# Kernel tuning notes

Hardware: AMD Instinct MI355X
Metric: run time of the kernel (lower is better)

The kernel has to match this reference:

```python
import jax, jax.numpy as jnp
import numpy as np

B, IN_C, L, D, K, DEPTH, OUT = 16, 3, 2048, 256, 8, 4, 1
F = L // 2 + 1
EPS = 1e-5


def _hilbert_basis_rfft(grid_size, k):
    # Hilbert matrix Z[i,j] = 1/(i+j+1), symmetric PSD; take top-k eigvecs.
    i = np.arange(grid_size, dtype=np.float64)
    Z = 1.0 / (i[:, None] + i[None, :] + 1.0)
    w, V = np.linalg.eigh(Z)
    idx = np.argsort(w)[::-1][:k]
    Vt = V.T[idx]                                   # (k, L)
    Phi_f = np.fft.rfft(Vt, n=grid_size, axis=-1)   # (k, L//2+1) complex
    return Phi_f.astype(np.complex64)


def setup_inputs() -> dict:
    key = jax.random.key(0)
    ks = jax.random.split(key, 10)
    phi = _hilbert_basis_rfft(L, K)
    s = 0.05
    return {
        "x": jax.random.normal(ks[0], (B, IN_C, L), jnp.float32),
        "lift_w": jax.random.normal(ks[1], (D, IN_C + 1), jnp.float32) * s,
        "lift_b": jax.random.normal(ks[2], (D,), jnp.float32) * s,
        "theta": jax.random.normal(ks[3], (DEPTH, K, D, D), jnp.float32) * (1.0 / np.sqrt(D)),
        "ln_gamma": jnp.ones((DEPTH, D), jnp.float32),
        "ln_beta": jnp.zeros((DEPTH, D), jnp.float32),
        "glu_val_w": jax.random.normal(ks[4], (DEPTH, D, D), jnp.float32) * (1.0 / np.sqrt(D)),
        "glu_val_b": jax.random.normal(ks[5], (DEPTH, D), jnp.float32) * s,
        "glu_gate_w": jax.random.normal(ks[6], (DEPTH, D, D), jnp.float32) * (1.0 / np.sqrt(D)),
        "glu_gate_b": jax.random.normal(ks[7], (DEPTH, D), jnp.float32) * s,
        "head_w": jax.random.normal(ks[8], (OUT, D), jnp.float32) * (1.0 / np.sqrt(D)),
        "head_b": jax.random.normal(ks[9], (OUT,), jnp.float32) * s,
        "phi_real": jnp.asarray(phi.real, jnp.float32),
        "phi_imag": jnp.asarray(phi.imag, jnp.float32),
    }


def _layernorm_channels(h, gamma, beta):
    # h: (b, d, t); normalize over channel dim d (matches LayerNorm on transposed input)
    mu = jnp.mean(h, axis=1, keepdims=True)
    var = jnp.mean(jnp.square(h - mu), axis=1, keepdims=True)
    z = (h - mu) * jax.lax.rsqrt(var + EPS)
    return z * gamma[None, :, None] + beta[None, :, None]


def reference(x, lift_w, lift_b, theta, ln_gamma, ln_beta,
              glu_val_w, glu_val_b, glu_gate_w, glu_gate_b,
              head_w, head_b, phi_real, phi_imag):
    phi = phi_real + 1j * phi_imag                      # (K, F) complex
    phi_c = jnp.conj(phi)
    # add grid coordinate channel
    coords = jnp.linspace(0.0, 1.0, L, dtype=x.dtype)
    coords = jnp.broadcast_to(coords[None, None, :], (x.shape[0], 1, L))
    h = jnp.concatenate([x, coords], axis=1)            # (b, in+1, L)
    # pointwise lift (Conv1d kernel_size=1, norm=Identity)
    h = jnp.einsum("oi,bit->bot", lift_w, h) + lift_b[None, :, None]
    for i in range(DEPTH):
        z = _layernorm_channels(h, ln_gamma[i], ln_beta[i])
        Xf = jnp.fft.rfft(z, axis=-1)                   # (b, d, F) complex64
        # Exploit FFT linearity: S = sum_{l,d} Theta[l,h,d] * irfft(Xf[b,d] * conj(Phi[l]))
        #                          = irfft( sum_{l,d} Theta[l,h,d]*conj(Phi[l,f]) * Xf[b,d,f] )
        W = jnp.einsum("lhd,lf->hdf", theta[i].astype(Xf.dtype), phi_c)  # (h, d, F)
        Sf = jnp.einsum("bdf,hdf->bhf", Xf, W)          # (b, h, F)
        S = jnp.fft.irfft(Sf, n=L, axis=-1)             # (b, h, L)
        V = jnp.einsum("od,bdt->bot", glu_val_w[i], S) + glu_val_b[i][None, :, None]
        G = jax.nn.sigmoid(jnp.einsum("od,bdt->bot", glu_gate_w[i], S) + glu_gate_b[i][None, :, None])
        h = h + V * G                                   # residual + GLU
    y = jnp.einsum("od,bdt->bot", head_w, h) + head_b[None, :, None]
    return y
```

## Files before the change

kernel.cpp:

```cpp
#include <hip/hip_runtime.h>
#include <math.h>

#define NB 16
#define CIN 3
#define LL 2048
#define DD 256
#define KK 8
#define NDEPTH 4
#define FF 1025
#define FFP 1032
#define FFS 1032
#define LOGL 11

typedef _Float16 half8 __attribute__((ext_vector_type(8)));
typedef _Float16 half2v __attribute__((ext_vector_type(2)));
typedef float f32x4 __attribute__((ext_vector_type(4)));

union H8 { half8 h8; unsigned int u[4]; uint4 q; };
union H2 { _Float16 h[2]; unsigned int u; half2v v; };
union PK4 { float2 f2[4]; uint4 q[2]; };

#if defined(__has_builtin)
#if __has_builtin(__builtin_amdgcn_fdot2)
#define HAS_FDOT2 1
#endif
#endif

__device__ inline float fdot2_acc(unsigned int a, unsigned int b, float c){
    H2 ua, ub; ua.u = a; ub.u = b;
#ifdef HAS_FDOT2
    return __builtin_amdgcn_fdot2(ua.v, ub.v, c, false);
#else
    return c + (float)ua.h[0]*(float)ub.h[0] + (float)ua.h[1]*(float)ub.h[1];
#endif
}

__device__ inline float2 cmul(const float2 a, const float2 b){
    return make_float2(a.x*b.x - a.y*b.y, a.x*b.y + a.y*b.x);
}

__global__ void twiddle_kernel(float2* __restrict__ tw){
    int j = blockIdx.x*blockDim.x + threadIdx.x;
    if (j < LL/2){
        double ang = -2.0*3.14159265358979323846*(double)j/(double)LL;
        tw[j] = make_float2((float)cos(ang), (float)sin(ang));
    }
}

__global__ void conv_w_kernel(const float* __restrict__ wv, const float* __restrict__ wg,
                              _Float16* __restrict__ Wf){
    int idx = blockIdx.x*256 + threadIdx.x;
    int layer = idx >> 17;
    int vg = (idx >> 16) & 1;
    int rem = idx & 65535;
    int o = rem >> 8, d = rem & 255;
    const float* src = (vg ? wg : wv) + ((size_t)layer << 16);
    float val = src[(o << 8) + d];
    size_t dst = ((((size_t)(layer*2+vg)*16 + (o>>4))*8 + (d>>5))*64
                  + (o&15) + 16*((d>>3)&3))*8 + (d&7);
    Wf[dst] = (_Float16)val;
}

__global__ void transpose_theta16_kernel(const float* __restrict__ in,
                                         unsigned int* __restrict__ out){
    __shared__ float tile[2][32][33];
    int m = blockIdx.z;
    int layer = m >> 2, lp = m & 3;
    int d0 = blockIdx.x*32, h0 = blockIdx.y*32;
    int tx = threadIdx.x & 31, ty = threadIdx.x >> 5;
    const float* src0 = in + ((size_t)layer*KK + 2*lp)*DD*DD;
    const float* src1 = src0 + (size_t)DD*DD;
    #pragma unroll
    for (int i = 0; i < 4; ++i){
        tile[0][ty + i*8][tx] = src0[(size_t)(h0 + ty + i*8)*DD + d0 + tx];
        tile[1][ty + i*8][tx] = src1[(size_t)(h0 + ty + i*8)*DD + d0 + tx];
    }
    __syncthreads();
    #pragma unroll
    for (int i = 0; i < 4; ++i){
        H2 p;
        p.h[0] = (_Float16)tile[0][tx][ty + i*8];
        p.h[1] = (_Float16)tile[1][tx][ty + i*8];
        out[((size_t)m*DD + d0 + ty + i*8)*DD + h0 + tx] = p.u;
    }
}

__global__ __launch_bounds__(256) void lift_ln_kernel(const float* __restrict__ x,
        const float* __restrict__ lw, const float* __restrict__ lb,
        const float* __restrict__ gamma, const float* __restrict__ beta,
        float* __restrict__ h, float* __restrict__ z){
    __shared__ float red[2][4][64];
    __shared__ float stat[2][64];
    __shared__ float gb[512];
    int tid = threadIdx.x;
    int t = tid & 63, dg = tid >> 6;
    int b = blockIdx.y;
    int tg = blockIdx.x*64 + t;
    gb[tid] = gamma[tid];
    gb[256 + tid] = beta[tid];
    const float* xb = x + (size_t)b*CIN*LL;
    float x0 = xb[tg], x1 = xb[LL + tg], x2 = xb[2*LL + tg];
    float coord = (float)tg * (1.0f/(LL-1));
    float hv[64];
    float s = 0.f, ss = 0.f;
    float* hp = h + (size_t)b*DD*LL + tg;
    #pragma unroll
    for (int j = 0; j < 64; ++j){
        int d = dg*64 + j;
        float4 w = *(const float4*)&lw[d*4];
        float v = lb[d];
        v = fmaf(w.x, x0, v); v = fmaf(w.y, x1, v);
        v = fmaf(w.z, x2, v); v = fmaf(w.w, coord, v);
        hv[j] = v;
        s += v; ss = fmaf(v, v, ss);
        hp[(size_t)d*LL] = v;
    }
    red[0][dg][t] = s; red[1][dg][t] = ss;
    __syncthreads();
    if (tid < 64){
        float S1 = red[0][0][tid] + red[0][1][tid] + red[0][2][tid] + red[0][3][tid];
        float S2 = red[1][0][tid] + red[1][1][tid] + red[1][2][tid] + red[1][3][tid];
        float mu = S1*(1.0f/DD);
        float var = S2*(1.0f/DD) - mu*mu;
        stat[0][tid] = mu;
        stat[1][tid] = rsqrtf(var + 1e-5f);
    }
    __syncthreads();
    float mu = stat[0][t], rs = stat[1][t];
    float* zp = z + (size_t)b*DD*LL + tg;
    #pragma unroll
    for (int j = 0; j < 64; ++j){
        int d = dg*64 + j;
        zp[(size_t)d*LL] = (hv[j] - mu)*rs*gb[d] + gb[256 + d];
    }
}

__global__ __launch_bounds__(256) void fft_fwd_pair_kernel(const float* __restrict__ in,
                                                           unsigned int* __restrict__ XfH,
                                                           const float2* __restrict__ tw){
    __shared__ float2 a[LL];
    int blk = blockIdx.x;
    const float* src0 = in + (size_t)(blk*2)*LL;
    const float* src1 = src0 + LL;
    int tid = threadIdx.x;
    #pragma unroll
    for (int i = 0; i < LL/256; ++i){
        int idx = tid + i*256;
        int rev = __brev((unsigned)idx) >> (32-LOGL);
        a[rev] = make_float2(src0[idx], src1[idx]);
    }
    __syncthreads();
    #pragma unroll
    for (int sp = 0; sp < 5; ++sp){
        const int s = sp*2;
        const int hs = 1 << s;
        #pragma unroll
        for (int gg = 0; gg < 2; ++gg){
            int g = tid + gg*256;
            int pos = g & (hs-1);
            int grp = g >> s;
            int q = (grp << (s+2)) + pos;
            float2 ws = tw[pos << (LOGL-1-s)];
            float2 w1 = tw[pos << (LOGL-2-s)];
            float2 w2 = tw[(pos+hs) << (LOGL-2-s)];
            float2 a0 = a[q], a1 = a[q+hs], a2 = a[q+2*hs], a3 = a[q+3*hs];
            float2 t1 = cmul(ws, a1), t3 = cmul(ws, a3);
            float2 x0 = make_float2(a0.x+t1.x, a0.y+t1.y);
            float2 x1 = make_float2(a0.x-t1.x, a0.y-t1.y);
            float2 x2 = make_float2(a2.x+t3.x, a2.y+t3.y);
            float2 x3 = make_float2(a2.x-t3.x, a2.y-t3.y);
            float2 u1 = cmul(w1, x2), u2 = cmul(w2, x3);
            a[q]       = make_float2(x0.x+u1.x, x0.y+u1.y);
            a[q+2*hs]  = make_float2(x0.x-u1.x, x0.y-u1.y);
            a[q+hs]    = make_float2(x1.x+u2.x, x1.y+u2.y);
            a[q+3*hs]  = make_float2(x1.x-u2.x, x1.y-u2.y);
        }
        __syncthreads();
    }
    #pragma unroll
    for (int jj = 0; jj < 4; ++jj){
        int j = tid + jj*256;
        float2 w = tw[j];
        float2 u = a[j];
        float2 v = cmul(w, a[j+1024]);
        a[j]      = make_float2(u.x+v.x, u.y+v.y);
        a[j+1024] = make_float2(u.x-v.x, u.y-v.y);
    }
    __syncthreads();
    unsigned int* dst0 = XfH + (size_t)(blk*2)*FFP;
    unsigned int* dst1 = dst0 + FFP;
    #pragma unroll
    for (int i = 0; i < 5; ++i){
        int f = tid + i*256;
        if (f <= 1024){
            int m = (LL - f) & (LL-1);
            float2 A = a[f], B = a[m];
            H2 p0, p1;
            p0.h[0] = (_Float16)(0.5f*(A.x + B.x));
            p0.h[1] = (_Float16)(0.5f*(A.y - B.y));
            p1.h[0] = (_Float16)(0.5f*(A.y + B.y));
            p1.h[1] = (_Float16)(0.5f*(B.x - A.x));
            dst0[f] = p0.u;
            dst1[f] = p1.u;
        }
    }
}

__global__ __launch_bounds__(256) void fft_inv_pair_kernel(const float2* __restrict__ Sf0,
                                                           unsigned int* __restrict__ Sfrag,
                                                           const float2* __restrict__ tw){
    __shared__ float2 a[LL];
    int blk = blockIdx.x;
    const float2* src0 = Sf0 + (size_t)(blk*2)*FFS;
    const float2* src1 = src0 + FFS;
    int tid = threadIdx.x;
    #pragma unroll
    for (int i = 0; i < LL/256; ++i){
        int idx = tid + i*256;
        float2 Y;
        if (idx <= 1024){
            float2 s0 = src0[idx], s1 = src1[idx];
            Y = make_float2(s0.x - s1.y, s0.y + s1.x);
        } else {
            int m = LL - idx;
            float2 s0 = src0[m], s1 = src1[m];
            Y = make_float2(s0.x + s1.y, s1.x - s0.y);
        }
        int rev = __brev((unsigned)idx) >> (32-LOGL);
        a[rev] = Y;
    }
    __syncthreads();
    #pragma unroll
    for (int sp = 0; sp < 5; ++sp){
        const int s = sp*2;
        const int hs = 1 << s;
        #pragma unroll
        for (int gg = 0; gg < 2; ++gg){
            int g = tid + gg*256;
            int pos = g & (hs-1);
            int grp = g >> s;
            int q = (grp << (s+2)) + pos;
            float2 ws = tw[pos << (LOGL-1-s)];  ws.y = -ws.y;
            float2 w1 = tw[pos << (LOGL-2-s)];  w1.y = -w1.y;
            float2 w2 = tw[(pos+hs) << (LOGL-2-s)]; w2.y = -w2.y;
            float2 a0v = a[q], a1v = a[q+hs], a2v = a[q+2*hs], a3v = a[q+3*hs];
            float2 t1 = cmul(ws, a1v), t3 = cmul(ws, a3v);
            float2 x0 = make_float2(a0v.x+t1.x, a0v.y+t1.y);
            float2 x1 = make_float2(a0v.x-t1.x, a0v.y-t1.y);
            float2 x2 = make_float2(a2v.x+t3.x, a2v.y+t3.y);
            float2 x3 = make_float2(a2v.x-t3.x, a2v.y-t3.y);
            float2 u1 = cmul(w1, x2), u2 = cmul(w2, x3);
            a[q]       = make_float2(x0.x+u1.x, x0.y+u1.y);
            a[q+2*hs]  = make_float2(x0.x-u1.x, x0.y-u1.y);
            a[q+hs]    = make_float2(x1.x+u2.x, x1.y+u2.y);
            a[q+3*hs]  = make_float2(x1.x-u2.x, x1.y-u2.y);
        }
        __syncthreads();
    }
    #pragma unroll
    for (int jj = 0; jj < 4; ++jj){
        int j = tid + jj*256;
        float2 w = tw[j]; w.y = -w.y;
        float2 u = a[j];
        float2 v = cmul(w, a[j+1024]);
        a[j]      = make_float2(u.x+v.x, u.y+v.y);
        a[j+1024] = make_float2(u.x-v.x, u.y-v.y);
    }
    __syncthreads();
    int b = blk >> 7, dl = (blk & 127)*2;
    int kc = dl >> 5, lq4 = (dl >> 3) & 3, jh = (dl & 7) >> 1;
    unsigned int* dst = Sfrag + ((size_t)(b*8 + kc)*128)*64*4;
    const float sc = 1.0f/(float)LL;
    #pragma unroll
    for (int i = 0; i < LL/256; ++i){
        int t = tid + i*256;
        float2 v = a[t];
        H2 p;
        p.h[0] = (_Float16)(v.x*sc);
        p.h[1] = (_Float16)(v.y*sc);
        dst[(((t>>4)*64) + (t&15) + 16*lq4)*4 + jh] = p.u;
    }
}

__global__ __launch_bounds__(512, 4) void spectral7_kernel(
    const unsigned int* __restrict__ XfH,
    const unsigned int* __restrict__ th16,
    const float* __restrict__ phr, const float* __restrict__ phim,
    float2* __restrict__ Sf0){
    __shared__ unsigned int Apairs[8*64*8];
    __shared__ unsigned int phi2[2][8][4];
    int tid = threadIdx.x;
    int w = tid >> 6, lane = tid & 63;
    int hc = w & 3, fh = w >> 2;
    int n = lane & 15, kp = lane >> 4;
    int f0 = blockIdx.x * 8;
    int h0 = blockIdx.y * 64;
    int h = h0 + hc*16 + n;

    if (tid < 32){
        int ff = tid >> 2, lp = tid & 3;
        H2 a, b;
        a.h[0] = (_Float16)phr[(2*lp)*FF + f0 + ff];
        a.h[1] = (_Float16)phr[(2*lp+1)*FF + f0 + ff];
        b.h[0] = (_Float16)(-phim[(2*lp)*FF + f0 + ff]);
        b.h[1] = (_Float16)(-phim[(2*lp+1)*FF + f0 + ff]);
        phi2[0][ff][lp] = a.u;
        phi2[1][ff][lp] = b.u;
    }

    f32x4 accre[4], accim[4];
    #pragma unroll
    for (int i = 0; i < 4; ++i){
        accre[i] = (f32x4){0.f,0.f,0.f,0.f};
        accim[i] = (f32x4){0.f,0.f,0.f,0.f};
    }

    for (int kc = 0; kc < 8; ++kc){
        unsigned int th_pk[4][8];
        #pragma unroll
        for (int lp = 0; lp < 4; ++lp)
            #pragma unroll
            for (int j = 0; j < 8; ++j)
                th_pk[lp][j] = th16[((size_t)lp*DD + kc*32 + kp*8 + j)*DD + h];

        __syncthreads();
        {
            int bb = tid & 15;
            int dd = tid >> 4;
            const uint4* src = (const uint4*)(XfH + ((size_t)(bb*DD + kc*32 + dd)*FFP + f0));
            uint4 v0 = src[0], v1 = src[1];
            int L = bb + 16*(dd >> 3), j = dd & 7;
            unsigned int vv[8] = {v0.x, v0.y, v0.z, v0.w, v1.x, v1.y, v1.z, v1.w};
            #pragma unroll
            for (int ff = 0; ff < 8; ++ff){
                int A = ff*2048 + L*32 + j*4;
                A ^= ((A >> 7) & 3) << 5;
                *(unsigned int*)((char*)Apairs + A) = vv[ff];
            }
        }
        __syncthreads();

        #pragma unroll
        for (int ffl = 0; ffl < 4; ++ffl){
            int ff = fh*4 + ffl;
            unsigned int pr2[4], pi2[4];
            #pragma unroll
            for (int lp = 0; lp < 4; ++lp){
                pr2[lp] = phi2[0][ff][lp];
                pi2[lp] = phi2[1][ff][lp];
            }
            int Ab = ff*2048 + lane*32;
            Ab ^= ((Ab >> 7) & 3) << 5;
            uint4 lo = *(const uint4*)((const char*)Apairs + Ab);
            uint4 hi = *(const uint4*)((const char*)Apairs + Ab + 16);
            unsigned int dw[8] = {lo.x, lo.y, lo.z, lo.w, hi.x, hi.y, hi.z, hi.w};
            H8 Are, Aim, Anim;
            #pragma unroll
            for (int k = 0; k < 4; ++k){
                Are.u[k]  = __builtin_amdgcn_perm(dw[2*k+1], dw[2*k], 0x05040100u);
                Aim.u[k]  = __builtin_amdgcn_perm(dw[2*k+1], dw[2*k], 0x07060302u);
                Anim.u[k] = Aim.u[k] ^ 0x80008000u;
            }
            float wre[8], wim[8];
            #pragma unroll
            for (int j = 0; j < 8; ++j){
                float re = 0.f, im = 0.f;
                #pragma unroll
                for (int lp = 0; lp < 4; ++lp){
                    re = fdot2_acc(th_pk[lp][j], pr2[lp], re);
                    im = fdot2_acc(th_pk[lp][j], pi2[lp], im);
                }
                wre[j] = re; wim[j] = im;
            }
            H8 Bre, Bim;
            #pragma unroll
            for (int j = 0; j < 8; ++j){
                Bre.h8[j] = (_Float16)wre[j];
                Bim.h8[j] = (_Float16)wim[j];
            }
            accre[ffl] = __builtin_amdgcn_mfma_f32_16x16x32_f16(Are.h8,  Bre.h8, accre[ffl], 0, 0, 0);
            accre[ffl] = __builtin_amdgcn_mfma_f32_16x16x32_f16(Anim.h8, Bim.h8, accre[ffl], 0, 0, 0);
            accim[ffl] = __builtin_amdgcn_mfma_f32_16x16x32_f16(Are.h8,  Bim.h8, accim[ffl], 0, 0, 0);
            accim[ffl] = __builtin_amdgcn_mfma_f32_16x16x32_f16(Aim.h8,  Bre.h8, accim[ffl], 0, 0, 0);
        }
    }
    #pragma unroll
    for (int r = 0; r < 4; ++r){
        int bb = kp*4 + r;
        PK4 pk;
        #pragma unroll
        for (int ffl = 0; ffl < 4; ++ffl)
            pk.f2[ffl] = make_float2(accre[ffl][r], accim[ffl][r]);
        uint4* dst = (uint4*)(Sf0 + ((size_t)(bb*DD) + h)*FFS + f0 + fh*4);
        dst[0] = pk.q[0]; dst[1] = pk.q[1];
    }
}

__global__ __launch_bounds__(256) void nyq_kernel(const unsigned int* __restrict__ XfH,
    const unsigned int* __restrict__ th16,
    const float* __restrict__ phr, const float* __restrict__ phim,
    float2* __restrict__ Sf0){
    __shared__ float2 red[256];
    int tid = threadIdx.x;
    int hb = blockIdx.x, b = blockIdx.y;
    int h = hb*16 + (tid & 15);
    int dp = tid >> 4;
    float pr[KK], pi[KK];
    #pragma unroll
    for (int l = 0; l < KK; ++l){ pr[l] = phr[l*FF + 1024]; pi[l] = -phim[l*FF + 1024]; }
    float2 acc = make_float2(0.f, 0.f);
    for (int j = 0; j < 16; ++j){
        int d = dp*16 + j;
        float wre = 0.f, wim = 0.f;
        #pragma unroll
        for (int lp = 0; lp < 4; ++lp){
            H2 t; t.u = th16[((size_t)lp*DD + d)*DD + h];
            float t0 = (float)t.h[0], t1 = (float)t.h[1];
            wre = fmaf(t0, pr[2*lp], fmaf(t1, pr[2*lp+1], wre));
            wim = fmaf(t0, pi[2*lp], fmaf(t1, pi[2*lp+1], wim));
        }
        H2 u; u.u = XfH[(size_t)(b*DD + d)*FFP + 1024];
        float2 x = make_float2((float)u.h[0], (float)u.h[1]);
        acc.x = fmaf(x.x, wre, fmaf(-x.y, wim, acc.x));
        acc.y = fmaf(x.x, wim, fmaf( x.y, wre, acc.y));
    }
    red[tid] = acc;
    __syncthreads();
    if (tid < 16){
        float2 s = make_float2(0.f, 0.f);
        #pragma unroll
        for (int k = 0; k < 16; ++k){ s.x += red[tid + k*16].x; s.y += red[tid + k*16].y; }
        Sf0[((size_t)b*DD + hb*16 + tid)*FFS + 1024] = s;
    }
}

template<int MODE>
__global__ __launch_bounds__(256, 2) void glu_mfma_kernel(
    const uint4* __restrict__ Sfrag,
    const uint4* __restrict__ WfL,
    const float* __restrict__ bv, const float* __restrict__ bg,
    float* __restrict__ h, float* __restrict__ outp,
    const float* __restrict__ aux1, const float* __restrict__ aux2){
    __shared__ float sb[1024];
    __shared__ float red[2][4][4][16];
    __shared__ float stat[2][4][16];
    int tid = threadIdx.x;
    int w = tid >> 6, lane = tid & 63;
    int tl = lane & 15, lq = lane >> 4;
    int b = blockIdx.y, tb4 = blockIdx.x;

    sb[tid] = bv[tid];
    sb[256 + tid] = bg[tid];
    sb[512 + tid] = aux1[tid];
    if (MODE == 0) sb[768 + tid] = aux2[tid];
    __syncthreads();

    f32x4 aV[4][4], aG[4][4];
    #pragma unroll
    for (int mt = 0; mt < 4; ++mt)
        #pragma unroll
        for (int nt = 0; nt < 4; ++nt){
            aV[mt][nt] = (f32x4){0.f,0.f,0.f,0.f};
            aG[mt][nt] = (f32x4){0.f,0.f,0.f,0.f};
        }

    for (int kc = 0; kc < 8; ++kc){
        H8 Bf[4];
        #pragma unroll
        for (int nt = 0; nt < 4; ++nt)
            Bf[nt].q = Sfrag[((size_t)(b*8 + kc)*128 + tb4*4 + nt)*64 + lane];
        H8 Av[4], Ag[4];
        #pragma unroll
        for (int mt = 0; mt < 4; ++mt){
            int ot = w*4 + mt;
            Av[mt].q = WfL[((size_t)(ot)*8 + kc)*64 + lane];
            Ag[mt].q = WfL[((size_t)(16 + ot)*8 + kc)*64 + lane];
        }
        #pragma unroll
        for (int mt = 0; mt < 4; ++mt)
            #pragma unroll
            for (int nt = 0; nt < 4; ++nt){
                aV[mt][nt] = __builtin_amdgcn_mfma_f32_16x16x32_f16(Av[mt].h8, Bf[nt].h8, aV[mt][nt], 0, 0, 0);
                aG[mt][nt] = __builtin_amdgcn_mfma_f32_16x16x32_f16(Ag[mt].h8, Bf[nt].h8, aG[mt][nt], 0, 0, 0);
            }
    }

    #pragma unroll
    for (int mt = 0; mt < 4; ++mt){
        #pragma unroll
        for (int r = 0; r < 4; ++r){
            int o = w*64 + mt*16 + lq*4 + r;
            float bvv = sb[o], bgv = sb[256 + o];
            float* hp = h + ((size_t)(b*DD + o))*LL + tb4*64 + tl;
            #pragma unroll
            for (int nt = 0; nt < 4; ++nt){
                float v = aV[mt][nt][r] + bvv;
                float g = aG[mt][nt][r] + bgv;
                g = 1.0f/(1.0f + __expf(-g));
                float cur = hp[nt*16] + v*g;
                if (MODE == 0) hp[nt*16] = cur;
                aV[mt][nt][r] = cur;
            }
        }
    }

    float s[4], ss[4];
    #pragma unroll
    for (int nt = 0; nt < 4; ++nt){ s[nt] = 0.f; ss[nt] = 0.f; }
    #pragma unroll
    for (int mt = 0; mt < 4; ++mt)
        #pragma unroll
        for (int r = 0; r < 4; ++r){
            int o = w*64 + mt*16 + lq*4 + r;
            float wo = (MODE == 0) ? 1.0f : sb[512 + o];
            #pragma unroll
            for (int nt = 0; nt < 4; ++nt){
                float cur = aV[mt][nt][r];
                if (MODE == 0){ s[nt] += cur; ss[nt] = fmaf(cur, cur, ss[nt]); }
                else { s[nt] = fmaf(wo, cur, s[nt]); }
            }
        }
    #pragma unroll
    for (int nt = 0; nt < 4; ++nt){
        s[nt] += __shfl_xor(s[nt], 16); s[nt] += __shfl_xor(s[nt], 32);
        if (MODE == 0){ ss[nt] += __shfl_xor(ss[nt], 16); ss[nt] += __shfl_xor(ss[nt], 32); }
    }
    if (lq == 0){
        #pragma unroll
        for (int nt = 0; nt < 4; ++nt){
            red[0][w][nt][tl] = s[nt];
            if (MODE == 0) red[1][w][nt][tl] = ss[nt];
        }
    }
    __syncthreads();
    if (MODE == 0){
        if (tid < 64){
            int nt = tid >> 4, t2 = tid & 15;
            float S1 = red[0][0][nt][t2] + red[0][1][nt][t2] + red[0][2][nt][t2] + red[0][3][nt][t2];
            float S2 = red[1][0][nt][t2] + red[1][1][nt][t2] + red[1][2][nt][t2] + red[1][3][nt][t2];
            float mu = S1*(1.0f/DD);
            float var = S2*(1.0f/DD) - mu*mu;
            stat[0][nt][t2] = mu;
            stat[1][nt][t2] = rsqrtf(var + 1e-5f);
        }
        __syncthreads();
        #pragma unroll
        for (int mt = 0; mt < 4; ++mt){
            #pragma unroll
            for (int r = 0; r < 4; ++r){
                int o = w*64 + mt*16 + lq*4 + r;
                float gam = sb[512 + o], bet = sb[768 + o];
                float* zp = outp + ((size_t)(b*DD + o))*LL + tb4*64 + tl;
                #pragma unroll
                for (int nt = 0; nt < 4; ++nt){
                    float zv = (aV[mt][nt][r] - stat[0][nt][tl])*stat[1][nt][tl]*gam + bet;
                    zp[nt*16] = zv;
                }
            }
        }
    } else {
        if (tid < 64){
            int nt = tid >> 4, t2 = tid & 15;
            float S1 = red[0][0][nt][t2] + red[0][1][nt][t2] + red[0][2][nt][t2] + red[0][3][nt][t2];
            outp[(size_t)b*LL + tb4*64 + tid] = S1 + aux2[0];
        }
    }
}

extern "C" void kernel_launch(void* const* d_in, const int* in_sizes, int n_in,
                              void* d_out, int out_size, void* d_ws, size_t ws_size,
                              hipStream_t stream){
    (void)in_sizes; (void)n_in; (void)out_size; (void)ws_size;
    const float* x      = (const float*)d_in[0];
    const float* lift_w = (const float*)d_in[1];
    const float* lift_b = (const float*)d_in[2];
    const float* theta  = (const float*)d_in[3];
    const float* ln_g   = (const float*)d_in[4];
    const float* ln_b   = (const float*)d_in[5];
    const float* gvw    = (const float*)d_in[6];
    const float* gvb    = (const float*)d_in[7];
    const float* ggw    = (const float*)d_in[8];
    const float* ggb    = (const float*)d_in[9];
    const float* hw     = (const float*)d_in[10];
    const float* hb     = (const float*)d_in[11];
    const float* phr    = (const float*)d_in[12];
    const float* phim   = (const float*)d_in[13];
    float* out = (float*)d_out;

    char* ws = (char*)d_ws;
    size_t off = 0;
    float2* tw  = (float2*)(ws + off); off += (size_t)(LL/2)*sizeof(float2);
    _Float16* Wf = (_Float16*)(ws + off); off += (size_t)NDEPTH*2*DD*DD*2;
    unsigned int* th16 = (unsigned int*)(ws + off); off += (size_t)NDEPTH*4*DD*DD*4;
    off = (off + 255) & ~(size_t)255;
    float*  h   = (float*)(ws + off);  off += (size_t)NB*DD*LL*4;
    float*  z   = (float*)(ws + off);  off += (size_t)NB*DD*LL*4;
    unsigned int* XfH = (unsigned int*)(ws + off); off += (size_t)NB*DD*FFP*4;
    unsigned int* Sfrag = XfH;
    off = (off + 255) & ~(size_t)255;
    float2* Sf0 = (float2*)(ws + off); off += (size_t)NB*DD*FFS*8;

    twiddle_kernel<<<4, 256, 0, stream>>>(tw);
    conv_w_kernel<<<(NDEPTH*2*DD*DD)/256, 256, 0, stream>>>(gvw, ggw, Wf);
    transpose_theta16_kernel<<<dim3(8,8,NDEPTH*4), 256, 0, stream>>>(theta, th16);
    lift_ln_kernel<<<dim3(LL/64, NB), 256, 0, stream>>>(x, lift_w, lift_b, ln_g, ln_b, h, z);

    for (int layer = 0; layer < NDEPTH; ++layer){
        const unsigned int* thL = th16 + (size_t)layer*4*DD*DD;
        const uint4* WfL = (const uint4*)(Wf + (size_t)layer*2*DD*DD);
        fft_fwd_pair_kernel<<<NB*DD/2, 256, 0, stream>>>(z, XfH, tw);
        spectral7_kernel<<<dim3(128,4), 512, 0, stream>>>(XfH, thL, phr, phim, Sf0);
        nyq_kernel<<<dim3(16,16), 256, 0, stream>>>(XfH, thL, phr, phim, Sf0);
        fft_inv_pair_kernel<<<NB*DD/2, 256, 0, stream>>>(Sf0, Sfrag, tw);
        if (layer < NDEPTH-1){
            glu_mfma_kernel<0><<<dim3(LL/64, NB), 256, 0, stream>>>(
                (const uint4*)Sfrag, WfL,
                gvb + layer*DD, ggb + layer*DD, h, z,
                ln_g + (layer+1)*DD, ln_b + (layer+1)*DD);
        } else {
            glu_mfma_kernel<1><<<dim3(LL/64, NB), 256, 0, stream>>>(
                (const uint4*)Sfrag, WfL,
                gvb + layer*DD, ggb + layer*DD, h, out, hw, hb);
        }
    }
}
```

Measured before the change: 538.3 us.

## Use radix-8 FFT stages, fp16 spectrum buffer, fold Nyquist bin into spectral kernel

```diff
diff --git a/kernel.cpp b/kernel.cpp
--- a/kernel.cpp
+++ b/kernel.cpp
@@ -9,7 +9,7 @@
 #define NDEPTH 4
 #define FF 1025
 #define FFP 1032
-#define FFS 1032
+#define FFSH 1040
 #define LOGL 11
 
 typedef _Float16 half8 __attribute__((ext_vector_type(8)));
@@ -18,7 +18,6 @@
 
 union H8 { half8 h8; unsigned int u[4]; uint4 q; };
 union H2 { _Float16 h[2]; unsigned int u; half2v v; };
-union PK4 { float2 f2[4]; uint4 q[2]; };
 
 #if defined(__has_builtin)
 #if __has_builtin(__builtin_amdgcn_fdot2)
@@ -37,6 +36,58 @@
 
 __device__ inline float2 cmul(const float2 a, const float2 b){
     return make_float2(a.x*b.x - a.y*b.y, a.x*b.y + a.y*b.x);
+}
+__device__ inline float2 cadd(const float2 a, const float2 b){ return make_float2(a.x+b.x, a.y+b.y); }
+__device__ inline float2 csub(const float2 a, const float2 b){ return make_float2(a.x-b.x, a.y-b.y); }
+__device__ inline float2 h2f(unsigned int u){ H2 t; t.u = u; return make_float2((float)t.h[0], (float)t.h[1]); }
+
+template<bool CONJ>
+__device__ inline void r8_stage(float2* a, const float2* __restrict__ tw, int g, int s){
+    const int hs = 1 << s;
+    int pos = g & (hs-1);
+    int grp = g >> s;
+    int q = (grp << (s+3)) + pos;
+    float2 ws = tw[pos << (LOGL-1-s)];
+    float2 w1 = tw[pos << (LOGL-2-s)];
+    float2 w2 = tw[(pos+hs) << (LOGL-2-s)];
+    float2 v0 = tw[pos << (LOGL-3-s)];
+    float2 v1 = tw[(pos+hs) << (LOGL-3-s)];
+    float2 v2 = tw[(pos+2*hs) << (LOGL-3-s)];
+    float2 v3 = tw[(pos+3*hs) << (LOGL-3-s)];
+    if (CONJ){ ws.y=-ws.y; w1.y=-w1.y; w2.y=-w2.y; v0.y=-v0.y; v1.y=-v1.y; v2.y=-v2.y; v3.y=-v3.y; }
+    float2 A0=a[q],      A1=a[q+hs],   A2=a[q+2*hs], A3=a[q+3*hs],
+           A4=a[q+4*hs], A5=a[q+5*hs], A6=a[q+6*hs], A7=a[q+7*hs];
+    float2 t;
+    t=cmul(ws,A1); float2 b0=cadd(A0,t), b1=csub(A0,t);
+    t=cmul(ws,A3); float2 b2=cadd(A2,t), b3=csub(A2,t);
+    t=cmul(ws,A5); float2 b4=cadd(A4,t), b5=csub(A4,t);
+    t=cmul(ws,A7); float2 b6=cadd(A6,t), b7=csub(A6,t);
+    t=cmul(w1,b2); float2 c0=cadd(b0,t), c2=csub(b0,t);
+    t=cmul(w2,b3); float2 c1=cadd(b1,t), c3=csub(b1,t);
+    t=cmul(w1,b6); float2 c4=cadd(b4,t), c6=csub(b4,t);
+    t=cmul(w2,b7); float2 c5=cadd(b5,t), c7=csub(b5,t);
+    t=cmul(v0,c4); a[q]      =cadd(c0,t); a[q+4*hs]=csub(c0,t);
+    t=cmul(v1,c5); a[q+hs]   =cadd(c1,t); a[q+5*hs]=csub(c1,t);
+    t=cmul(v2,c6); a[q+2*hs] =cadd(c2,t); a[q+6*hs]=csub(c2,t);
+    t=cmul(v3,c7); a[q+3*hs] =cadd(c3,t); a[q+7*hs]=csub(c3,t);
+}
+
+template<bool CONJ>
+__device__ inline void r4_final(float2* a, const float2* __restrict__ tw, int g){
+    int pos = g;
+    float2 ws = tw[pos << 1];
+    float2 w1 = tw[pos];
+    float2 w2 = tw[pos + 512];
+    if (CONJ){ ws.y=-ws.y; w1.y=-w1.y; w2.y=-w2.y; }
+    float2 a0 = a[pos], a1 = a[pos+512], a2 = a[pos+1024], a3 = a[pos+1536];
+    float2 t1 = cmul(ws, a1), t3 = cmul(ws, a3);
+    float2 x0 = cadd(a0,t1), x1 = csub(a0,t1);
+    float2 x2 = cadd(a2,t3), x3 = csub(a2,t3);
+    float2 u1 = cmul(w1, x2), u2 = cmul(w2, x3);
+    a[pos]      = cadd(x0,u1);
+    a[pos+1024] = csub(x0,u1);
+    a[pos+512]  = cadd(x1,u2);
+    a[pos+1536] = csub(x1,u2);
 }
 
 __global__ void twiddle_kernel(float2* __restrict__ tw){
@@ -150,42 +201,11 @@
         a[rev] = make_float2(src0[idx], src1[idx]);
     }
     __syncthreads();
-    #pragma unroll
-    for (int sp = 0; sp < 5; ++sp){
-        const int s = sp*2;
-        const int hs = 1 << s;
-        #pragma unroll
-        for (int gg = 0; gg < 2; ++gg){
-            int g = tid + gg*256;
-            int pos = g & (hs-1);
-            int grp = g >> s;
-            int q = (grp << (s+2)) + pos;
-            float2 ws = tw[pos << (LOGL-1-s)];
-            float2 w1 = tw[pos << (LOGL-2-s)];
-            float2 w2 = tw[(pos+hs) << (LOGL-2-s)];
-            float2 a0 = a[q], a1 = a[q+hs], a2 = a[q+2*hs], a3 = a[q+3*hs];
-            float2 t1 = cmul(ws, a1), t3 = cmul(ws, a3);
-            float2 x0 = make_float2(a0.x+t1.x, a0.y+t1.y);
-            float2 x1 = make_float2(a0.x-t1.x, a0.y-t1.y);
-            float2 x2 = make_float2(a2.x+t3.x, a2.y+t3.y);
-            float2 x3 = make_float2(a2.x-t3.x, a2.y-t3.y);
-            float2 u1 = cmul(w1, x2), u2 = cmul(w2, x3);
-            a[q]       = make_float2(x0.x+u1.x, x0.y+u1.y);
-            a[q+2*hs]  = make_float2(x0.x-u1.x, x0.y-u1.y);
-            a[q+hs]    = make_float2(x1.x+u2.x, x1.y+u2.y);
-            a[q+3*hs]  = make_float2(x1.x-u2.x, x1.y-u2.y);
-        }
-        __syncthreads();
-    }
-    #pragma unroll
-    for (int jj = 0; jj < 4; ++jj){
-        int j = tid + jj*256;
-        float2 w = tw[j];
-        float2 u = a[j];
-        float2 v = cmul(w, a[j+1024]);
-        a[j]      = make_float2(u.x+v.x, u.y+v.y);
-        a[j+1024] = make_float2(u.x-v.x, u.y-v.y);
-    }
+    r8_stage<false>(a, tw, tid, 0);  __syncthreads();
+    r8_stage<false>(a, tw, tid, 3);  __syncthreads();
+    r8_stage<false>(a, tw, tid, 6);  __syncthreads();
+    r4_final<false>(a, tw, tid);
+    r4_final<false>(a, tw, tid + 256);
     __syncthreads();
     unsigned int* dst0 = XfH + (size_t)(blk*2)*FFP;
     unsigned int* dst1 = dst0 + FFP;
@@ -204,89 +224,61 @@
             dst1[f] = p1.u;
         }
     }
-}
-
-__global__ __launch_bounds__(256) void fft_inv_pair_kernel(const float2* __restrict__ Sf0,
+    if (tid < 7){
+        dst0[1025 + tid] = 0u;
+        dst1[1025 + tid] = 0u;
+    }
+}
+
+__global__ __launch_bounds__(256) void fft_inv_pair_kernel(const unsigned int* __restrict__ SfH,
                                                            unsigned int* __restrict__ Sfrag,
                                                            const float2* __restrict__ tw){
     __shared__ float2 a[LL];
     int blk = blockIdx.x;
-    const float2* src0 = Sf0 + (size_t)(blk*2)*FFS;
-    const float2* src1 = src0 + FFS;
+    const unsigned int* a0 = SfH + (size_t)(blk*2)*FFSH;
+    const unsigned int* b0 = a0 + FFSH;
     int tid = threadIdx.x;
     #pragma unroll
     for (int i = 0; i < LL/256; ++i){
         int idx = tid + i*256;
         float2 Y;
         if (idx <= 1024){
-            float2 s0 = src0[idx], s1 = src1[idx];
+            float2 s0 = h2f(a0[idx]), s1 = h2f(b0[idx]);
             Y = make_float2(s0.x - s1.y, s0.y + s1.x);
         } else {
             int m = LL - idx;
-            float2 s0 = src0[m], s1 = src1[m];
+            float2 s0 = h2f(a0[m]), s1 = h2f(b0[m]);
             Y = make_float2(s0.x + s1.y, s1.x - s0.y);
         }
         int rev = __brev((unsigned)idx) >> (32-LOGL);
         a[rev] = Y;
     }
     __syncthreads();
-    #pragma unroll
-    for (int sp = 0; sp < 5; ++sp){
-        const int s = sp*2;
-        const int hs = 1 << s;
-        #pragma unroll
-        for (int gg = 0; gg < 2; ++gg){
-            int g = tid + gg*256;
-            int pos = g & (hs-1);
-            int grp = g >> s;
-            int q = (grp << (s+2)) + pos;
-            float2 ws = tw[pos << (LOGL-1-s)];  ws.y = -ws.y;
-            float2 w1 = tw[pos << (LOGL-2-s)];  w1.y = -w1.y;
-            float2 w2 = tw[(pos+hs) << (LOGL-2-s)]; w2.y = -w2.y;
-            float2 a0v = a[q], a1v = a[q+hs], a2v = a[q+2*hs], a3v = a[q+3*hs];
-            float2 t1 = cmul(ws, a1v), t3 = cmul(ws, a3v);
-            float2 x0 = make_float2(a0v.x+t1.x, a0v.y+t1.y);
-            float2 x1 = make_float2(a0v.x-t1.x, a0v.y-t1.y);
-            float2 x2 = make_float2(a2v.x+t3.x, a2v.y+t3.y);
-            float2 x3 = make_float2(a2v.x-t3.x, a2v.y-t3.y);
-            float2 u1 = cmul(w1, x2), u2 = cmul(w2, x3);
-            a[q]       = make_float2(x0.x+u1.x, x0.y+u1.y);
-            a[q+2*hs]  = make_float2(x0.x-u1.x, x0.y-u1.y);
-            a[q+hs]    = make_float2(x1.x+u2.x, x1.y+u2.y);
-            a[q+3*hs]  = make_float2(x1.x-u2.x, x1.y-u2.y);
-        }
-        __syncthreads();
-    }
-    #pragma unroll
-    for (int jj = 0; jj < 4; ++jj){
-        int j = tid + jj*256;
-        float2 w = tw[j]; w.y = -w.y;
-        float2 u = a[j];
-        float2 v = cmul(w, a[j+1024]);
-        a[j]      = make_float2(u.x+v.x, u.y+v.y);
-        a[j+1024] = make_float2(u.x-v.x, u.y-v.y);
-    }
+    r8_stage<true>(a, tw, tid, 0);  __syncthreads();
+    r8_stage<true>(a, tw, tid, 3);  __syncthreads();
+    r8_stage<true>(a, tw, tid, 6);  __syncthreads();
+    r4_final<true>(a, tw, tid);
+    r4_final<true>(a, tw, tid + 256);
     __syncthreads();
     int b = blk >> 7, dl = (blk & 127)*2;
     int kc = dl >> 5, lq4 = (dl >> 3) & 3, jh = (dl & 7) >> 1;
     unsigned int* dst = Sfrag + ((size_t)(b*8 + kc)*128)*64*4;
-    const float sc = 1.0f/(float)LL;
     #pragma unroll
     for (int i = 0; i < LL/256; ++i){
         int t = tid + i*256;
         float2 v = a[t];
         H2 p;
-        p.h[0] = (_Float16)(v.x*sc);
-        p.h[1] = (_Float16)(v.y*sc);
+        p.h[0] = (_Float16)v.x;
+        p.h[1] = (_Float16)v.y;
         dst[(((t>>4)*64) + (t&15) + 16*lq4)*4 + jh] = p.u;
     }
 }
 
-__global__ __launch_bounds__(512, 4) void spectral7_kernel(
+__global__ __launch_bounds__(512, 4) void spectral8_kernel(
     const unsigned int* __restrict__ XfH,
     const unsigned int* __restrict__ th16,
     const float* __restrict__ phr, const float* __restrict__ phim,
-    float2* __restrict__ Sf0){
+    unsigned int* __restrict__ SfH){
     __shared__ unsigned int Apairs[8*64*8];
     __shared__ unsigned int phi2[2][8][4];
     int tid = threadIdx.x;
@@ -299,11 +291,12 @@
 
     if (tid < 32){
         int ff = tid >> 2, lp = tid & 3;
+        int fi = f0 + ff; if (fi > 1024) fi = 1024;
         H2 a, b;
-        a.h[0] = (_Float16)phr[(2*lp)*FF + f0 + ff];
-        a.h[1] = (_Float16)phr[(2*lp+1)*FF + f0 + ff];
-        b.h[0] = (_Float16)(-phim[(2*lp)*FF + f0 + ff]);
-        b.h[1] = (_Float16)(-phim[(2*lp+1)*FF + f0 + ff]);
+        a.h[0] = (_Float16)phr[(2*lp)*FF + fi];
+        a.h[1] = (_Float16)phr[(2*lp+1)*FF + fi];
+        b.h[0] = (_Float16)(-phim[(2*lp)*FF + fi]);
+        b.h[1] = (_Float16)(-phim[(2*lp+1)*FF + fi]);
         phi2[0][ff][lp] = a.u;
         phi2[1][ff][lp] = b.u;
     }
@@ -384,53 +377,20 @@
             accim[ffl] = __builtin_amdgcn_mfma_f32_16x16x32_f16(Aim.h8,  Bre.h8, accim[ffl], 0, 0, 0);
         }
     }
+    const float sc = 1.0f/(float)LL;
     #pragma unroll
     for (int r = 0; r < 4; ++r){
         int bb = kp*4 + r;
-        PK4 pk;
-        #pragma unroll
-        for (int ffl = 0; ffl < 4; ++ffl)
-            pk.f2[ffl] = make_float2(accre[ffl][r], accim[ffl][r]);
-        uint4* dst = (uint4*)(Sf0 + ((size_t)(bb*DD) + h)*FFS + f0 + fh*4);
-        dst[0] = pk.q[0]; dst[1] = pk.q[1];
-    }
-}
-
-__global__ __launch_bounds__(256) void nyq_kernel(const unsigned int* __restrict__ XfH,
-    const unsigned int* __restrict__ th16,
-    const float* __restrict__ phr, const float* __restrict__ phim,
-    float2* __restrict__ Sf0){
-    __shared__ float2 red[256];
-    int tid = threadIdx.x;
-    int hb = blockIdx.x, b = blockIdx.y;
-    int h = hb*16 + (tid & 15);
-    int dp = tid >> 4;
-    float pr[KK], pi[KK];
-    #pragma unroll
-    for (int l = 0; l < KK; ++l){ pr[l] = phr[l*FF + 1024]; pi[l] = -phim[l*FF + 1024]; }
-    float2 acc = make_float2(0.f, 0.f);
-    for (int j = 0; j < 16; ++j){
-        int d = dp*16 + j;
-        float wre = 0.f, wim = 0.f;
-        #pragma unroll
-        for (int lp = 0; lp < 4; ++lp){
-            H2 t; t.u = th16[((size_t)lp*DD + d)*DD + h];
-            float t0 = (float)t.h[0], t1 = (float)t.h[1];
-            wre = fmaf(t0, pr[2*lp], fmaf(t1, pr[2*lp+1], wre));
-            wim = fmaf(t0, pi[2*lp], fmaf(t1, pi[2*lp+1], wim));
-        }
-        H2 u; u.u = XfH[(size_t)(b*DD + d)*FFP + 1024];
-        float2 x = make_float2((float)u.h[0], (float)u.h[1]);
-        acc.x = fmaf(x.x, wre, fmaf(-x.y, wim, acc.x));
-        acc.y = fmaf(x.x, wim, fmaf( x.y, wre, acc.y));
-    }
-    red[tid] = acc;
-    __syncthreads();
-    if (tid < 16){
-        float2 s = make_float2(0.f, 0.f);
-        #pragma unroll
-        for (int k = 0; k < 16; ++k){ s.x += red[tid + k*16].x; s.y += red[tid + k*16].y; }
-        Sf0[((size_t)b*DD + hb*16 + tid)*FFS + 1024] = s;
+        unsigned int pk[4];
+        #pragma unroll
+        for (int ffl = 0; ffl < 4; ++ffl){
+            H2 p;
+            p.h[0] = (_Float16)(accre[ffl][r]*sc);
+            p.h[1] = (_Float16)(accim[ffl][r]*sc);
+            pk[ffl] = p.u;
+        }
+        uint4 val = make_uint4(pk[0], pk[1], pk[2], pk[3]);
+        *(uint4*)(SfH + ((size_t)(bb*DD) + h)*FFSH + f0 + fh*4) = val;
     }
 }
 
@@ -598,7 +558,7 @@
     unsigned int* XfH = (unsigned int*)(ws + off); off += (size_t)NB*DD*FFP*4;
     unsigned int* Sfrag = XfH;
     off = (off + 255) & ~(size_t)255;
-    float2* Sf0 = (float2*)(ws + off); off += (size_t)NB*DD*FFS*8;
+    unsigned int* SfH = (unsigned int*)(ws + off); off += (size_t)NB*DD*FFSH*4;
 
     twiddle_kernel<<<4, 256, 0, stream>>>(tw);
     conv_w_kernel<<<(NDEPTH*2*DD*DD)/256, 256, 0, stream>>>(gvw, ggw, Wf);
@@ -609,9 +569,8 @@
         const unsigned int* thL = th16 + (size_t)layer*4*DD*DD;
         const uint4* WfL = (const uint4*)(Wf + (size_t)layer*2*DD*DD);
         fft_fwd_pair_kernel<<<NB*DD/2, 256, 0, stream>>>(z, XfH, tw);
-        spectral7_kernel<<<dim3(128,4), 512, 0, stream>>>(XfH, thL, phr, phim, Sf0);
-        nyq_kernel<<<dim3(16,16), 256, 0, stream>>>(XfH, thL, phr, phim, Sf0);
-        fft_inv_pair_kernel<<<NB*DD/2, 256, 0, stream>>>(Sf0, Sfrag, tw);
+        spectral8_kernel<<<dim3(129,4), 512, 0, stream>>>(XfH, thL, phr, phim, SfH);
+        fft_inv_pair_kernel<<<NB*DD/2, 256, 0, stream>>>(SfH, Sfrag, tw);
         if (layer < NDEPTH-1){
             glu_mfma_kernel<0><<<dim3(LL/64, NB), 256, 0, stream>>>(
                 (const uint4*)Sfrag, WfL,
```

Measured after the change: 568.7 us. +5.6%, slower.
